# Optimization experiments

Hardware: AMD Instinct MI355X
Metric: run time of the kernel (lower is better)

The kernel has to match this reference:

```python
import jax, jax.numpy as jnp
import numpy as np

B, S, D_IN, D_HID, D_OUT, PE_DIM = 8, 4096, 1024, 1024, 1024, 16


def sinusoidal_embeddings(batch_size, seq_len, dim):
    positions = jnp.arange(seq_len)[:, None].astype(jnp.float32)
    div_term = jnp.exp(jnp.arange(0, dim, 2).astype(jnp.float32) * (-jnp.log(10000.0) / dim))
    pe = jnp.zeros((seq_len, dim), dtype=jnp.float32)
    pe = pe.at[:, 0::2].set(jnp.sin(positions * div_term))
    pe = pe.at[:, 1::2].set(jnp.cos(positions * div_term))
    return jnp.broadcast_to(pe, (batch_size, seq_len, dim))


def setup_inputs() -> dict:
    key = jax.random.key(0)
    ks = jax.random.split(key, 8)
    d_cat = D_IN + PE_DIM
    # a_logit drawn so that sigmoid(a_logit) lands in the stable decay range [0.9, 0.999]
    u = jax.random.uniform(ks[1], (D_HID,), minval=0.9, maxval=0.999)
    a_logit = jnp.log(u) - jnp.log1p(-u)  # logit
    scale_in = 1.0 / np.sqrt(d_cat)
    scale_h = 1.0 / np.sqrt(D_HID)
    return {
        "x": jax.random.normal(ks[0], (B, S, D_IN), dtype=jnp.float32),
        "a_logit": a_logit.astype(jnp.float32),
        "W_dx": jax.random.normal(ks[2], (d_cat, D_OUT), dtype=jnp.float32) * scale_in,
        "b_dx": jnp.zeros((D_OUT,), dtype=jnp.float32),
        "W_in": jax.random.normal(ks[3], (d_cat, D_HID), dtype=jnp.float32) * scale_in,
        "b_in": jnp.zeros((D_HID,), dtype=jnp.float32),
        "W_out": jax.random.normal(ks[4], (D_HID, D_OUT), dtype=jnp.float32) * scale_h,
        "b_out": jnp.zeros((D_OUT,), dtype=jnp.float32),
    }


def reference(x, a_logit, W_dx, b_dx, W_in, b_in, W_out, b_out):
    batch, seq, _ = x.shape
    a = jax.nn.sigmoid(a_logit)  # (d_hidden,)
    # rnn_pos_embedding: concat 16-dim sinusoidal PE
    xc = jnp.concatenate([x, sinusoidal_embeddings(batch, seq, PE_DIM)], axis=-1)
    dx = xc @ W_dx + b_dx  # (B, S, d_out)
    u = xc @ W_in + b_in  # (B, S, d_hidden)
    # rnn_norm_input
    u = jnp.sqrt(1.0 - a ** 2) * u
    u = jnp.transpose(u, (1, 0, 2))  # (S, B, d_hidden)

    def step(h, xt):
        h = a * h + xt
        return h, h

    init = jnp.zeros((batch, a.shape[0]), dtype=x.dtype)
    _, h = jax.lax.scan(step, init, u)
    h = jnp.transpose(h, (1, 0, 2))  # (B, S, d_hidden)
    return (dx + h @ W_out + b_out) / 2
```

## Files before the change

### kernel.cpp

```cpp
#include <hip/hip_runtime.h>
#include <hip/hip_bf16.h>
#include <math.h>

#define B_DIM 8
#define S_DIM 4096
#define DIN   1024
#define DHID  1024
#define DOUT  1024
#define KCAT  1040
#define KC    1056
#define MTOT  (B_DIM*S_DIM)
#define NCHUNK 32
#define LCHUNK 128

#define GBK 32

typedef __attribute__((ext_vector_type(8))) short bf16x8;
typedef __attribute__((ext_vector_type(4))) float f32x4;
typedef __attribute__((ext_vector_type(4))) unsigned short u16x4;

__device__ __forceinline__ unsigned short f2bf(float f) {
  union { float f; unsigned u; } v; v.f = f;
  unsigned r = v.u + 0x7fffu + ((v.u >> 16) & 1u);
  return (unsigned short)(r >> 16);
}
__device__ __forceinline__ float bf2f(unsigned short h) {
  union { unsigned u; float f; } v; v.u = ((unsigned)h) << 16;
  return v.f;
}

#define GLOAD16(g, l)                                                         \
  __builtin_amdgcn_global_load_lds(                                           \
      (const __attribute__((address_space(1))) void*)(g),                     \
      (__attribute__((address_space(3))) void*)(l), 16, 0, 0)


__global__ void prep_a_kernel(const float* __restrict__ logit,
                              float* __restrict__ avec, float* __restrict__ svec) {
  int d = blockIdx.x * 256 + threadIdx.x;
  if (d >= DHID) return;
  float a = 1.f / (1.f + expf(-logit[d]));
  avec[d] = a;
  svec[d] = sqrtf(fmaxf(0.f, 1.f - a * a));
}

__global__ __launch_bounds__(256) void transpose_cast_kernel(
    const float* __restrict__ W, unsigned short* __restrict__ Wt,
    int Ksrc, int KCdst) {
  __shared__ float tile[32][33];
  const int N = 1024;
  int kb = blockIdx.x * 32, nb = blockIdx.y * 32;
  int tx = threadIdx.x & 31, ty = threadIdx.x >> 5;
#pragma unroll
  for (int r = 0; r < 32; r += 8) {
    int k = kb + ty + r;
    tile[ty + r][tx] = (k < Ksrc) ? W[(size_t)k * N + nb + tx] : 0.f;
  }
  __syncthreads();
#pragma unroll
  for (int r = 0; r < 32; r += 8) {
    int n = nb + ty + r;
    Wt[(size_t)n * KCdst + kb + tx] = f2bf(tile[tx][ty + r]);
  }
}

__global__ __launch_bounds__(256) void build_xc_kernel(
    const float* __restrict__ x, unsigned short* __restrict__ xc) {
  int gid = blockIdx.x * 256 + threadIdx.x;
  if (gid >= MTOT * (KC / 4)) return;
  int row = gid / (KC / 4);
  int g = gid - row * (KC / 4);
  int col0 = g * 4;
  u16x4 val;
  if (col0 < DIN) {
    const float4 xv = *(const float4*)(x + (size_t)row * DIN + col0);
    val.x = f2bf(xv.x); val.y = f2bf(xv.y); val.z = f2bf(xv.z); val.w = f2bf(xv.w);
  } else {
    int t = row & (S_DIM - 1);
#pragma unroll
    for (int e = 0; e < 4; e++) {
      int col = col0 + e;
      float v = 0.f;
      if (col < KCAT) {
        int j = col - DIN;
        int i = j >> 1;
        float div = expf(-(float)i * 1.1512925465f);
        float arg = (float)t * div;
        v = (j & 1) ? cosf(arg) : sinf(arg);
      }
      val[e] = f2bf(v);
    }
  }
  *(u16x4*)(xc + (size_t)row * KC + col0) = val;
}


__device__ __forceinline__ bf16x8 lds_frag(const unsigned short* buf, int row, int s) {
  int c = (row << 2) | ((s ^ (row >> 1)) & 3);
  return *(const bf16x8*)(buf + (c << 3));
}

__device__ __forceinline__ void gemm_pipe(
    const unsigned short* __restrict__ A,
    const unsigned short* __restrict__ Bt,
    int lda, int kt, int arow0, int brow0,
    unsigned short (*lA)[8192], unsigned short (*lB)[8192],
    f32x4 acc[8][4]) {
  const int tid = threadIdx.x;
  const int lane = tid & 63, w = tid >> 6;
  const int wrow = w >> 2, wcol = w & 3;
  const int rl = lane & 15, s = lane >> 4;

  int cA0 = w * 128 + lane;        int g0 = cA0 ^ ((cA0 >> 3) & 3);
  int cA1 = w * 128 + 64 + lane;   int g1 = cA1 ^ ((cA1 >> 3) & 3);
  const unsigned short* pA0 = A  + (size_t)(arow0 + (g0 >> 2)) * lda + (g0 & 3) * 8;
  const unsigned short* pA1 = A  + (size_t)(arow0 + (g1 >> 2)) * lda + (g1 & 3) * 8;
  const unsigned short* pB0 = Bt + (size_t)(brow0 + (g0 >> 2)) * lda + (g0 & 3) * 8;
  const unsigned short* pB1 = Bt + (size_t)(brow0 + (g1 >> 2)) * lda + (g1 & 3) * 8;
  const int lo0 = (w * 128) * 8;
  const int lo1 = (w * 128 + 64) * 8;

#define STAGE(t)                                                              \
  do { int _b = (t) & 3; size_t _k = (size_t)(t) * GBK;                       \
    GLOAD16(pA0 + _k, &lA[_b][lo0]);                                          \
    GLOAD16(pA1 + _k, &lA[_b][lo1]);                                          \
    GLOAD16(pB0 + _k, &lB[_b][lo0]);                                          \
    GLOAD16(pB1 + _k, &lB[_b][lo1]);                                          \
  } while (0)

  STAGE(0); STAGE(1); STAGE(2);
  asm volatile("s_waitcnt vmcnt(8)" ::: "memory");
  __builtin_amdgcn_s_barrier();
  __builtin_amdgcn_sched_barrier(0);

  for (int t = 0; t < kt; ++t) {
    if (t + 3 < kt) STAGE(t + 3);
    const unsigned short* bufA = lA[t & 3];
    const unsigned short* bufB = lB[t & 3];
    bf16x8 bf[4], af[4];
#pragma unroll
    for (int n = 0; n < 4; n++) bf[n] = lds_frag(bufB, wcol * 64 + n * 16 + rl, s);
#pragma unroll
    for (int m = 0; m < 4; m++) af[m] = lds_frag(bufA, wrow * 128 + m * 16 + rl, s);
    __builtin_amdgcn_s_setprio(1);
#pragma unroll
    for (int m = 0; m < 4; m++)
#pragma unroll
      for (int n = 0; n < 4; n++)
        acc[m][n] = __builtin_amdgcn_mfma_f32_16x16x32_bf16(af[m], bf[n], acc[m][n], 0, 0, 0);
    __builtin_amdgcn_s_setprio(0);
#pragma unroll
    for (int m = 0; m < 4; m++) af[m] = lds_frag(bufA, wrow * 128 + 64 + m * 16 + rl, s);
    __builtin_amdgcn_s_setprio(1);
#pragma unroll
    for (int m = 0; m < 4; m++)
#pragma unroll
      for (int n = 0; n < 4; n++)
        acc[m + 4][n] = __builtin_amdgcn_mfma_f32_16x16x32_bf16(af[m], bf[n], acc[m + 4][n], 0, 0, 0);
    __builtin_amdgcn_s_setprio(0);
    if (t < kt - 1) {
      if (t + 3 < kt)      asm volatile("s_waitcnt vmcnt(8)" ::: "memory");
      else if (t + 2 < kt) asm volatile("s_waitcnt vmcnt(4)" ::: "memory");
      else                 asm volatile("s_waitcnt vmcnt(0)" ::: "memory");
      __builtin_amdgcn_s_barrier();
      __builtin_amdgcn_sched_barrier(0);
    }
  }
  asm volatile("s_waitcnt vmcnt(0)" ::: "memory");
  __builtin_amdgcn_s_barrier();
  __builtin_amdgcn_sched_barrier(0);
#undef STAGE
}

__global__ __launch_bounds__(512, 2) void gemm_u_kernel(
    const unsigned short* __restrict__ xc, const unsigned short* __restrict__ Wtin,
    const float* __restrict__ b_in, const float* __restrict__ svec,
    unsigned short* __restrict__ u) {
  __shared__ __align__(16) unsigned short lA[4][8192];
  __shared__ __align__(16) unsigned short lB[4][8192];
  f32x4 acc[8][4];
  const f32x4 z = {0.f, 0.f, 0.f, 0.f};
#pragma unroll
  for (int i = 0; i < 8; i++)
#pragma unroll
    for (int n = 0; n < 4; n++) acc[i][n] = z;

  int bid = blockIdx.x;
  int swz = (bid & 7) * 64 + (bid >> 3);
  int bcol = swz >> 7, brow = swz & 127;

  gemm_pipe(xc, Wtin, KC, KC / GBK, brow * 256, bcol * 256, lA, lB, acc);

  const int lane = threadIdx.x & 63, w = threadIdx.x >> 6;
  const int wrow = w >> 2, wcol = w & 3;
  const int rl = lane & 15, s = lane >> 4;
  const int colb = bcol * 256 + wcol * 64 + rl;
  const int rowb = brow * 256 + wrow * 128 + s * 4;
#pragma unroll
  for (int n = 0; n < 4; n++) {
    int col = colb + n * 16;
    float bi = b_in[col], sv = svec[col];
#pragma unroll
    for (int i = 0; i < 8; i++) {
#pragma unroll
      for (int r = 0; r < 4; r++) {
        int row = rowb + i * 16 + r;
        u[(size_t)row * DHID + col] = f2bf((acc[i][n][r] + bi) * sv);
      }
    }
  }
}

__global__ __launch_bounds__(512, 2) void gemm_out_kernel(
    const unsigned short* __restrict__ xc, const unsigned short* __restrict__ Wtdx,
    const unsigned short* __restrict__ h, const unsigned short* __restrict__ Wtout,
    const float* __restrict__ b_dx, const float* __restrict__ b_out,
    float* __restrict__ out) {
  __shared__ __align__(16) unsigned short lA[4][8192];
  __shared__ __align__(16) unsigned short lB[4][8192];
  f32x4 acc[8][4];
  const f32x4 z = {0.f, 0.f, 0.f, 0.f};
#pragma unroll
  for (int i = 0; i < 8; i++)
#pragma unroll
    for (int n = 0; n < 4; n++) acc[i][n] = z;

  int bid = blockIdx.x;
  int swz = (bid & 7) * 64 + (bid >> 3);
  int bcol = swz >> 7, brow = swz & 127;

  gemm_pipe(xc, Wtdx, KC, KC / GBK, brow * 256, bcol * 256, lA, lB, acc);
  gemm_pipe(h, Wtout, DHID, DHID / GBK, brow * 256, bcol * 256, lA, lB, acc);

  const int lane = threadIdx.x & 63, w = threadIdx.x >> 6;
  const int wrow = w >> 2, wcol = w & 3;
  const int rl = lane & 15, s = lane >> 4;
  const int colb = bcol * 256 + wcol * 64 + rl;
  const int rowb = brow * 256 + wrow * 128 + s * 4;
#pragma unroll
  for (int n = 0; n < 4; n++) {
    int col = colb + n * 16;
    float bb = b_dx[col] + b_out[col];
#pragma unroll
    for (int i = 0; i < 8; i++) {
#pragma unroll
      for (int r = 0; r < 4; r++) {
        int row = rowb + i * 16 + r;
        out[(size_t)row * DOUT + col] = 0.5f * (acc[i][n][r] + bb);
      }
    }
  }
}


__global__ __launch_bounds__(256) void scan1_kernel(
    const float* __restrict__ avec, unsigned short* __restrict__ uh,
    float* __restrict__ carry) {
  int blk = blockIdx.x;
  int d = (blk & 3) * 256 + threadIdx.x;
  int c = (blk >> 2) & 31;
  int b = blk >> 7;
  float a = avec[d];
  unsigned short* p = uh + ((size_t)(b * S_DIM + c * LCHUNK)) * DHID + d;
  float h = 0.f;
#pragma unroll 4
  for (int t = 0; t < LCHUNK; t++) {
    float uv = bf2f(p[(size_t)t * DHID]);
    h = fmaf(a, h, uv);
    p[(size_t)t * DHID] = f2bf(h);
  }
  carry[((size_t)b * NCHUNK + c) * DHID + d] = h;
}

__global__ __launch_bounds__(256) void scan2_kernel(
    const float* __restrict__ avec, const float* __restrict__ carry,
    float* __restrict__ Hprev) {
  int gid = blockIdx.x * 256 + threadIdx.x;
  int b = gid >> 10, d = gid & 1023;
  float a = avec[d];
  float aL = a;
#pragma unroll
  for (int i = 0; i < 7; i++) aL *= aL;
  float H = 0.f;
#pragma unroll
  for (int c = 0; c < NCHUNK; c++) {
    size_t idx = ((size_t)b * NCHUNK + c) * DHID + d;
    Hprev[idx] = H;
    H = aL * H + carry[idx];
  }
}

__global__ __launch_bounds__(256) void scan3_kernel(
    const float* __restrict__ avec, unsigned short* __restrict__ uh,
    const float* __restrict__ Hprev) {
  int blk = blockIdx.x;
  int d = (blk & 3) * 256 + threadIdx.x;
  int c = (blk >> 2) & 31;
  int b = blk >> 7;
  float Hp = Hprev[((size_t)b * NCHUNK + c) * DHID + d];
  if (Hp == 0.f) return;
  float a = avec[d];
  float pw = a;
  unsigned short* p = uh + ((size_t)(b * S_DIM + c * LCHUNK)) * DHID + d;
#pragma unroll 4
  for (int t = 0; t < LCHUNK; t++) {
    float hv = bf2f(p[(size_t)t * DHID]) + pw * Hp;
    p[(size_t)t * DHID] = f2bf(hv);
    pw *= a;
  }
}


extern "C" void kernel_launch(void* const* d_in, const int* in_sizes, int n_in,
                              void* d_out, int out_size, void* d_ws, size_t ws_size,
                              hipStream_t stream) {
  const float* x       = (const float*)d_in[0];
  const float* a_logit = (const float*)d_in[1];
  const float* W_dx    = (const float*)d_in[2];
  const float* b_dx    = (const float*)d_in[3];
  const float* W_in    = (const float*)d_in[4];
  const float* b_in    = (const float*)d_in[5];
  const float* W_out   = (const float*)d_in[6];
  const float* b_out   = (const float*)d_in[7];
  float* out = (float*)d_out;

  char* ws = (char*)d_ws;
  size_t off = 0;
  auto alloc = [&](size_t bytes) {
    void* p = ws + off;
    off += (bytes + 255) & ~(size_t)255;
    return p;
  };
  unsigned short* xc    = (unsigned short*)alloc((size_t)MTOT * KC * 2);
  unsigned short* Wtdx  = (unsigned short*)alloc((size_t)DOUT * KC * 2);
  unsigned short* Wtin  = (unsigned short*)alloc((size_t)DHID * KC * 2);
  unsigned short* Wtout = (unsigned short*)alloc((size_t)DOUT * DHID * 2);
  unsigned short* uh    = (unsigned short*)alloc((size_t)MTOT * DHID * 2);
  float* carry = (float*)alloc((size_t)B_DIM * NCHUNK * DHID * 4);
  float* Hprev = (float*)alloc((size_t)B_DIM * NCHUNK * DHID * 4);
  float* avec  = (float*)alloc(DHID * 4);
  float* svec  = (float*)alloc(DHID * 4);
  (void)ws_size; (void)in_sizes; (void)n_in; (void)out_size;

  prep_a_kernel<<<4, 256, 0, stream>>>(a_logit, avec, svec);
  transpose_cast_kernel<<<dim3(KC / 32, 32), 256, 0, stream>>>(W_dx, Wtdx, KCAT, KC);
  transpose_cast_kernel<<<dim3(KC / 32, 32), 256, 0, stream>>>(W_in, Wtin, KCAT, KC);
  transpose_cast_kernel<<<dim3(32, 32), 256, 0, stream>>>(W_out, Wtout, DHID, DHID);
  build_xc_kernel<<<(MTOT * (KC / 4) + 255) / 256, 256, 0, stream>>>(x, xc);

  gemm_u_kernel<<<512, 512, 0, stream>>>(xc, Wtin, b_in, svec, uh);

  scan1_kernel<<<B_DIM * NCHUNK * 4, 256, 0, stream>>>(avec, uh, carry);
  scan2_kernel<<<32, 256, 0, stream>>>(avec, carry, Hprev);
  scan3_kernel<<<B_DIM * NCHUNK * 4, 256, 0, stream>>>(avec, uh, Hprev);

  gemm_out_kernel<<<512, 512, 0, stream>>>(xc, Wtdx, uh, Wtout, b_dx, b_out, out);
}
```

Before: 415.7 us.

## Restructure GEMM pipeline to BK=64 double-buffer with interleaved quadrant MFMA and vectorize scans

Replaces the 4-stage BK=32 GEMM pipeline with a 2-stage BK=64 double buffer split into row halves. It uses an 8-slot XOR swizzle and issues MFMAs in four quadrants, with the next stage's global-to-LDS loads interleaved between them under extra barriers. KC padding grows to 1088 so the K loop divides by 64. The scan kernels now have each thread process 4 hidden channels with vector loads and stores, cutting the launch to a quarter of the blocks. The aim is to halve barrier count per K and improve latency hiding. The cost is extra padded K work and more barriers per iteration.

```diff
diff --git a/kernel.cpp b/kernel.cpp
--- a/kernel.cpp
+++ b/kernel.cpp
@@ -8,12 +8,10 @@
 #define DHID  1024
 #define DOUT  1024
 #define KCAT  1040
-#define KC    1056
+#define KC    1088
 #define MTOT  (B_DIM*S_DIM)
 #define NCHUNK 32
 #define LCHUNK 128
-
-#define GBK 32
 
 typedef __attribute__((ext_vector_type(8))) short bf16x8;
 typedef __attribute__((ext_vector_type(4))) float f32x4;
@@ -33,6 +31,10 @@
   __builtin_amdgcn_global_load_lds(                                           \
       (const __attribute__((address_space(1))) void*)(g),                     \
       (__attribute__((address_space(3))) void*)(l), 16, 0, 0)
+
+#define BAR()   __builtin_amdgcn_s_barrier()
+#define LGKM0() do { asm volatile("s_waitcnt lgkmcnt(0)" ::: "memory");       \
+                     __builtin_amdgcn_sched_barrier(0); } while (0)
 
 
 __global__ void prep_a_kernel(const float* __restrict__ logit,
@@ -95,89 +97,113 @@
 }
 
 
-__device__ __forceinline__ bf16x8 lds_frag(const unsigned short* buf, int row, int s) {
-  int c = (row << 2) | ((s ^ (row >> 1)) & 3);
-  return *(const bf16x8*)(buf + (c << 3));
-}
-
-__device__ __forceinline__ void gemm_pipe(
+__device__ __forceinline__ bf16x8 frag(const unsigned short* hb, int row, int slot) {
+  int ph = slot ^ (row & 7);
+  return *(const bf16x8*)(hb + (size_t)row * 64 + ph * 8);
+}
+
+__device__ __forceinline__ void gemm_pipe2(
     const unsigned short* __restrict__ A,
     const unsigned short* __restrict__ Bt,
     int lda, int kt, int arow0, int brow0,
-    unsigned short (*lA)[8192], unsigned short (*lB)[8192],
+    unsigned short (*lA)[2][8192], unsigned short (*lB)[2][8192],
     f32x4 acc[8][4]) {
   const int tid = threadIdx.x;
   const int lane = tid & 63, w = tid >> 6;
   const int wrow = w >> 2, wcol = w & 3;
   const int rl = lane & 15, s = lane >> 4;
 
-  int cA0 = w * 128 + lane;        int g0 = cA0 ^ ((cA0 >> 3) & 3);
-  int cA1 = w * 128 + 64 + lane;   int g1 = cA1 ^ ((cA1 >> 3) & 3);
-  const unsigned short* pA0 = A  + (size_t)(arow0 + (g0 >> 2)) * lda + (g0 & 3) * 8;
-  const unsigned short* pA1 = A  + (size_t)(arow0 + (g1 >> 2)) * lda + (g1 & 3) * 8;
-  const unsigned short* pB0 = Bt + (size_t)(brow0 + (g0 >> 2)) * lda + (g0 & 3) * 8;
-  const unsigned short* pB1 = Bt + (size_t)(brow0 + (g1 >> 2)) * lda + (g1 & 3) * 8;
-  const int lo0 = (w * 128) * 8;
-  const int lo1 = (w * 128 + 64) * 8;
-
-#define STAGE(t)                                                              \
-  do { int _b = (t) & 3; size_t _k = (size_t)(t) * GBK;                       \
-    GLOAD16(pA0 + _k, &lA[_b][lo0]);                                          \
-    GLOAD16(pA1 + _k, &lA[_b][lo1]);                                          \
-    GLOAD16(pB0 + _k, &lB[_b][lo0]);                                          \
-    GLOAD16(pB1 + _k, &lB[_b][lo1]);                                          \
-  } while (0)
-
-  STAGE(0); STAGE(1); STAGE(2);
+  const int c1 = tid, c2 = tid + 512;
+  const int r1 = c1 >> 3, sl1 = (c1 & 7) ^ (r1 & 7);
+  const int r2 = c2 >> 3, sl2 = (c2 & 7) ^ (r2 & 7);
+  const unsigned short* pA1 = A + (size_t)(arow0 + r1) * lda + sl1 * 8;
+  const unsigned short* pA2 = A + (size_t)(arow0 + r2) * lda + sl2 * 8;
+  const unsigned short* pB1 = Bt + (size_t)(brow0 + r1) * lda + sl1 * 8;
+  const unsigned short* pB2 = Bt + (size_t)(brow0 + r2) * lda + sl2 * 8;
+  const size_t hstep = (size_t)128 * lda;
+
+#define STG_A(t, h) do { size_t _o = (size_t)(t) * 64 + (size_t)(h) * hstep;  \
+    int _b = (t) & 1;                                                         \
+    GLOAD16(pA1 + _o, &lA[_b][h][(size_t)c1 * 8]);                            \
+    GLOAD16(pA2 + _o, &lA[_b][h][(size_t)c2 * 8]); } while (0)
+#define STG_B(t, h) do { size_t _o = (size_t)(t) * 64 + (size_t)(h) * hstep;  \
+    int _b = (t) & 1;                                                         \
+    GLOAD16(pB1 + _o, &lB[_b][h][(size_t)c1 * 8]);                            \
+    GLOAD16(pB2 + _o, &lB[_b][h][(size_t)c2 * 8]); } while (0)
+
+#define MFMA_Q(MH, NH, BB)                                                    \
+  __builtin_amdgcn_s_setprio(1);                                              \
+  _Pragma("unroll") for (int mq = 0; mq < 4; mq++)                            \
+    _Pragma("unroll") for (int nq = 0; nq < 2; nq++)                          \
+      _Pragma("unroll") for (int kk = 0; kk < 2; kk++)                        \
+        acc[(MH)*4 + mq][(NH)*2 + nq] =                                       \
+            __builtin_amdgcn_mfma_f32_16x16x32_bf16(                          \
+                a[mq][kk], BB[nq][kk], acc[(MH)*4 + mq][(NH)*2 + nq], 0, 0, 0);\
+  __builtin_amdgcn_s_setprio(0);
+
+  STG_B(0, 0); STG_B(0, 1); STG_A(0, 0); STG_A(0, 1);
+  STG_B(1, 0); STG_B(1, 1); STG_A(1, 0); STG_A(1, 1);
   asm volatile("s_waitcnt vmcnt(8)" ::: "memory");
-  __builtin_amdgcn_s_barrier();
-  __builtin_amdgcn_sched_barrier(0);
-
+  BAR();
+
+  const int br = (wcol & 1) * 64;
   for (int t = 0; t < kt; ++t) {
-    if (t + 3 < kt) STAGE(t + 3);
-    const unsigned short* bufA = lA[t & 3];
-    const unsigned short* bufB = lB[t & 3];
-    bf16x8 bf[4], af[4];
-#pragma unroll
-    for (int n = 0; n < 4; n++) bf[n] = lds_frag(bufB, wcol * 64 + n * 16 + rl, s);
-#pragma unroll
-    for (int m = 0; m < 4; m++) af[m] = lds_frag(bufA, wrow * 128 + m * 16 + rl, s);
-    __builtin_amdgcn_s_setprio(1);
-#pragma unroll
-    for (int m = 0; m < 4; m++)
-#pragma unroll
-      for (int n = 0; n < 4; n++)
-        acc[m][n] = __builtin_amdgcn_mfma_f32_16x16x32_bf16(af[m], bf[n], acc[m][n], 0, 0, 0);
-    __builtin_amdgcn_s_setprio(0);
-#pragma unroll
-    for (int m = 0; m < 4; m++) af[m] = lds_frag(bufA, wrow * 128 + 64 + m * 16 + rl, s);
-    __builtin_amdgcn_s_setprio(1);
-#pragma unroll
-    for (int m = 0; m < 4; m++)
-#pragma unroll
-      for (int n = 0; n < 4; n++)
-        acc[m + 4][n] = __builtin_amdgcn_mfma_f32_16x16x32_bf16(af[m], bf[n], acc[m + 4][n], 0, 0, 0);
-    __builtin_amdgcn_s_setprio(0);
-    if (t < kt - 1) {
-      if (t + 3 < kt)      asm volatile("s_waitcnt vmcnt(8)" ::: "memory");
-      else if (t + 2 < kt) asm volatile("s_waitcnt vmcnt(4)" ::: "memory");
-      else                 asm volatile("s_waitcnt vmcnt(0)" ::: "memory");
-      __builtin_amdgcn_s_barrier();
-      __builtin_amdgcn_sched_barrier(0);
-    }
-  }
-  asm volatile("s_waitcnt vmcnt(0)" ::: "memory");
-  __builtin_amdgcn_s_barrier();
-  __builtin_amdgcn_sched_barrier(0);
-#undef STAGE
+    const bool st = (t + 2) < kt;
+    const unsigned short* Ac = &lA[t & 1][wrow][0];
+    const unsigned short* Bc = &lB[t & 1][wcol >> 1][0];
+    bf16x8 a[4][2], b0[2][2], b1[2][2];
+
+#pragma unroll
+    for (int mq = 0; mq < 4; mq++)
+#pragma unroll
+      for (int kk = 0; kk < 2; kk++)
+        a[mq][kk] = frag(Ac, mq * 16 + rl, kk * 4 + s);
+#pragma unroll
+    for (int nq = 0; nq < 2; nq++)
+#pragma unroll
+      for (int kk = 0; kk < 2; kk++)
+        b0[nq][kk] = frag(Bc, br + nq * 16 + rl, kk * 4 + s);
+    BAR(); LGKM0();
+    MFMA_Q(0, 0, b0);
+    BAR();
+
+#pragma unroll
+    for (int nq = 0; nq < 2; nq++)
+#pragma unroll
+      for (int kk = 0; kk < 2; kk++)
+        b1[nq][kk] = frag(Bc, br + 32 + nq * 16 + rl, kk * 4 + s);
+    BAR(); LGKM0();
+    MFMA_Q(0, 1, b1);
+    BAR();
+
+#pragma unroll
+    for (int mq = 0; mq < 4; mq++)
+#pragma unroll
+      for (int kk = 0; kk < 2; kk++)
+        a[mq][kk] = frag(Ac, 64 + mq * 16 + rl, kk * 4 + s);
+    if (st) { STG_B(t + 2, 0); STG_B(t + 2, 1); }
+    BAR(); LGKM0();
+    MFMA_Q(1, 1, b1);
+    BAR();
+
+    if (st) { STG_A(t + 2, 0); STG_A(t + 2, 1); }
+    BAR();
+    MFMA_Q(1, 0, b0);
+    if (st) { asm volatile("s_waitcnt vmcnt(8)" ::: "memory"); }
+    else    { asm volatile("s_waitcnt vmcnt(0)" ::: "memory"); }
+    BAR();
+  }
+#undef STG_A
+#undef STG_B
+#undef MFMA_Q
 }
 
 __global__ __launch_bounds__(512, 2) void gemm_u_kernel(
     const unsigned short* __restrict__ xc, const unsigned short* __restrict__ Wtin,
     const float* __restrict__ b_in, const float* __restrict__ svec,
     unsigned short* __restrict__ u) {
-  __shared__ __align__(16) unsigned short lA[4][8192];
-  __shared__ __align__(16) unsigned short lB[4][8192];
+  __shared__ __align__(16) unsigned short lA[2][2][8192];
+  __shared__ __align__(16) unsigned short lB[2][2][8192];
   f32x4 acc[8][4];
   const f32x4 z = {0.f, 0.f, 0.f, 0.f};
 #pragma unroll
@@ -189,7 +215,7 @@
   int swz = (bid & 7) * 64 + (bid >> 3);
   int bcol = swz >> 7, brow = swz & 127;
 
-  gemm_pipe(xc, Wtin, KC, KC / GBK, brow * 256, bcol * 256, lA, lB, acc);
+  gemm_pipe2(xc, Wtin, KC, KC / 64, brow * 256, bcol * 256, lA, lB, acc);
 
   const int lane = threadIdx.x & 63, w = threadIdx.x >> 6;
   const int wrow = w >> 2, wcol = w & 3;
@@ -216,8 +242,8 @@
     const unsigned short* __restrict__ h, const unsigned short* __restrict__ Wtout,
     const float* __restrict__ b_dx, const float* __restrict__ b_out,
     float* __restrict__ out) {
-  __shared__ __align__(16) unsigned short lA[4][8192];
-  __shared__ __align__(16) unsigned short lB[4][8192];
+  __shared__ __align__(16) unsigned short lA[2][2][8192];
+  __shared__ __align__(16) unsigned short lB[2][2][8192];
   f32x4 acc[8][4];
   const f32x4 z = {0.f, 0.f, 0.f, 0.f};
 #pragma unroll
@@ -229,8 +255,8 @@
   int swz = (bid & 7) * 64 + (bid >> 3);
   int bcol = swz >> 7, brow = swz & 127;
 
-  gemm_pipe(xc, Wtdx, KC, KC / GBK, brow * 256, bcol * 256, lA, lB, acc);
-  gemm_pipe(h, Wtout, DHID, DHID / GBK, brow * 256, bcol * 256, lA, lB, acc);
+  gemm_pipe2(xc, Wtdx, KC, KC / 64, brow * 256, bcol * 256, lA, lB, acc);
+  gemm_pipe2(h, Wtout, DHID, DHID / 64, brow * 256, bcol * 256, lA, lB, acc);
 
   const int lane = threadIdx.x & 63, w = threadIdx.x >> 6;
   const int wrow = w >> 2, wcol = w & 3;
@@ -256,20 +282,23 @@
 __global__ __launch_bounds__(256) void scan1_kernel(
     const float* __restrict__ avec, unsigned short* __restrict__ uh,
     float* __restrict__ carry) {
-  int blk = blockIdx.x;
-  int d = (blk & 3) * 256 + threadIdx.x;
-  int c = (blk >> 2) & 31;
-  int b = blk >> 7;
-  float a = avec[d];
-  unsigned short* p = uh + ((size_t)(b * S_DIM + c * LCHUNK)) * DHID + d;
-  float h = 0.f;
+  int b = blockIdx.x >> 5, c = blockIdx.x & 31;
+  int d0 = threadIdx.x * 4;
+  float4 a4 = *(const float4*)(avec + d0);
+  unsigned short* p = uh + ((size_t)(b * S_DIM + c * LCHUNK)) * DHID + d0;
+  float h0 = 0.f, h1 = 0.f, h2 = 0.f, h3 = 0.f;
 #pragma unroll 4
   for (int t = 0; t < LCHUNK; t++) {
-    float uv = bf2f(p[(size_t)t * DHID]);
-    h = fmaf(a, h, uv);
-    p[(size_t)t * DHID] = f2bf(h);
-  }
-  carry[((size_t)b * NCHUNK + c) * DHID + d] = h;
+    u16x4 v = *(u16x4*)(p + (size_t)t * DHID);
+    h0 = fmaf(a4.x, h0, bf2f(v.x));
+    h1 = fmaf(a4.y, h1, bf2f(v.y));
+    h2 = fmaf(a4.z, h2, bf2f(v.z));
+    h3 = fmaf(a4.w, h3, bf2f(v.w));
+    v.x = f2bf(h0); v.y = f2bf(h1); v.z = f2bf(h2); v.w = f2bf(h3);
+    *(u16x4*)(p + (size_t)t * DHID) = v;
+  }
+  float4 cv = {h0, h1, h2, h3};
+  *(float4*)(carry + ((size_t)b * NCHUNK + c) * DHID + d0) = cv;
 }
 
 __global__ __launch_bounds__(256) void scan2_kernel(
@@ -293,20 +322,22 @@
 __global__ __launch_bounds__(256) void scan3_kernel(
     const float* __restrict__ avec, unsigned short* __restrict__ uh,
     const float* __restrict__ Hprev) {
-  int blk = blockIdx.x;
-  int d = (blk & 3) * 256 + threadIdx.x;
-  int c = (blk >> 2) & 31;
-  int b = blk >> 7;
-  float Hp = Hprev[((size_t)b * NCHUNK + c) * DHID + d];
-  if (Hp == 0.f) return;
-  float a = avec[d];
-  float pw = a;
-  unsigned short* p = uh + ((size_t)(b * S_DIM + c * LCHUNK)) * DHID + d;
+  int b = blockIdx.x >> 5, c = blockIdx.x & 31;
+  int d0 = threadIdx.x * 4;
+  float4 Hp = *(const float4*)(Hprev + ((size_t)b * NCHUNK + c) * DHID + d0);
+  if (Hp.x == 0.f && Hp.y == 0.f && Hp.z == 0.f && Hp.w == 0.f) return;
+  float4 a4 = *(const float4*)(avec + d0);
+  float p0 = a4.x * Hp.x, p1 = a4.y * Hp.y, p2 = a4.z * Hp.z, p3 = a4.w * Hp.w;
+  unsigned short* p = uh + ((size_t)(b * S_DIM + c * LCHUNK)) * DHID + d0;
 #pragma unroll 4
   for (int t = 0; t < LCHUNK; t++) {
-    float hv = bf2f(p[(size_t)t * DHID]) + pw * Hp;
-    p[(size_t)t * DHID] = f2bf(hv);
-    pw *= a;
+    u16x4 v = *(u16x4*)(p + (size_t)t * DHID);
+    v.x = f2bf(bf2f(v.x) + p0);
+    v.y = f2bf(bf2f(v.y) + p1);
+    v.z = f2bf(bf2f(v.z) + p2);
+    v.w = f2bf(bf2f(v.w) + p3);
+    *(u16x4*)(p + (size_t)t * DHID) = v;
+    p0 *= a4.x; p1 *= a4.y; p2 *= a4.z; p3 *= a4.w;
   }
 }
 
@@ -350,9 +381,9 @@
 
   gemm_u_kernel<<<512, 512, 0, stream>>>(xc, Wtin, b_in, svec, uh);
 
-  scan1_kernel<<<B_DIM * NCHUNK * 4, 256, 0, stream>>>(avec, uh, carry);
+  scan1_kernel<<<B_DIM * NCHUNK, 256, 0, stream>>>(avec, uh, carry);
   scan2_kernel<<<32, 256, 0, stream>>>(avec, carry, Hprev);
-  scan3_kernel<<<B_DIM * NCHUNK * 4, 256, 0, stream>>>(avec, uh, Hprev);
+  scan3_kernel<<<B_DIM * NCHUNK, 256, 0, stream>>>(avec, uh, Hprev);
 
   gemm_out_kernel<<<512, 512, 0, stream>>>(xc, Wtdx, uh, Wtout, b_dx, b_out, out);
 }
```

Result: faster. 339.6 us (-18.3%).
